# Performance work log

Measured on AMD Instinct MI355X. Metric: run time of the kernel, lower is better.

The kernel has to match this reference:

```python
import jax, jax.numpy as jnp
import numpy as np

EMB = 1024
HEADS = 16
HEAD_DIM = EMB // HEADS


def setup_inputs() -> dict:
    key = jax.random.key(0)
    ks = jax.random.split(key, 9)
    s = 1.0 / np.sqrt(EMB)
    x = jax.random.normal(ks[0], (4, 2048, EMB), dtype=jnp.float32)
    Wq = jax.random.uniform(ks[1], (EMB, EMB), minval=-s, maxval=s, dtype=jnp.float32)
    bq = jax.random.uniform(ks[2], (EMB,), minval=-s, maxval=s, dtype=jnp.float32)
    Wk = jax.random.uniform(ks[3], (EMB, EMB), minval=-s, maxval=s, dtype=jnp.float32)
    bk = jax.random.uniform(ks[4], (EMB,), minval=-s, maxval=s, dtype=jnp.float32)
    Wv = jax.random.uniform(ks[5], (EMB, EMB), minval=-s, maxval=s, dtype=jnp.float32)
    bv = jax.random.uniform(ks[6], (EMB,), minval=-s, maxval=s, dtype=jnp.float32)
    Wo = jax.random.uniform(ks[7], (EMB, EMB), minval=-s, maxval=s, dtype=jnp.float32)
    bo = jax.random.uniform(ks[8], (EMB,), minval=-s, maxval=s, dtype=jnp.float32)
    return {"x": x, "Wq": Wq, "bq": bq, "Wk": Wk, "bk": bk, "Wv": Wv, "bv": bv, "Wo": Wo, "bo": bo}


def reference(x, Wq, bq, Wk, bk, Wv, bv, Wo, bo):
    B, S, E = x.shape
    # QKV projections (torch Linear: y = x W^T + b)
    q = x @ Wq.T + bq
    k = x @ Wk.T + bk
    v = x @ Wv.T + bv
    # split heads -> [B, H, S, Dh]
    q = q.reshape(B, S, HEADS, HEAD_DIM).transpose(0, 2, 1, 3)
    k = k.reshape(B, S, HEADS, HEAD_DIM).transpose(0, 2, 1, 3)
    v = v.reshape(B, S, HEADS, HEAD_DIM).transpose(0, 2, 1, 3)
    # NOTE: module scales by 1/sqrt(emb_size), NOT 1/sqrt(head_dim)
    scale = 1.0 / jnp.sqrt(jnp.asarray(E, dtype=x.dtype))
    energy = jnp.einsum('bhqd,bhkd->bhqk', q, k) * scale
    attention = jax.nn.softmax(energy, axis=-1)
    out = jnp.einsum('bhqk,bhkd->bhqd', attention, v)
    out = out.transpose(0, 2, 1, 3).reshape(B, S, E)
    return out @ Wo.T + bo
```

## Files before the change

### kernel.cpp

```cpp
#include <hip/hip_runtime.h>


typedef __bf16 bf16;
typedef __attribute__((ext_vector_type(4))) short shortx4;
typedef __attribute__((ext_vector_type(8))) short short8;
typedef __attribute__((ext_vector_type(4))) float floatx4;
typedef __attribute__((ext_vector_type(2))) unsigned int uintx2;
typedef __attribute__((ext_vector_type(4))) unsigned int uintx4;

#define MFMA16(a, b, c) __builtin_amdgcn_mfma_f32_16x16x32_bf16((a), (b), (c), 0, 0, 0)

#define LDS_STRIDE 56

__device__ __forceinline__ float fast_exp2(float x) {
    float r;
    asm("v_exp_f32 %0, %1" : "=v"(r) : "v"(x));
    return r;
}
__device__ __forceinline__ unsigned int cvt_pk_bf16(float lo, float hi) {
    unsigned int r;
    asm("v_cvt_pk_bf16_f32 %0, %1, %2" : "=v"(r) : "v"(lo), "v"(hi));
    return r;
}

__device__ __forceinline__ void async16(const bf16* __restrict__ g, short* l) {
    __builtin_amdgcn_global_load_lds((const __attribute__((address_space(1))) void*)g,
                                     (__attribute__((address_space(3))) void*)l, 16, 0, 0);
}

__device__ __forceinline__ short8 frag8(const bf16* __restrict__ p) {
    return *(const short8*)p;
}
__device__ __forceinline__ short8 frag8(const float* __restrict__ p) {
    const floatx4 a = *(const floatx4*)p;
    const floatx4 b = *(const floatx4*)(p + 4);
    short8 r;
#pragma unroll
    for (int j = 0; j < 4; j++) {
        r[j]     = __builtin_bit_cast(short, (bf16)a[j]);
        r[4 + j] = __builtin_bit_cast(short, (bf16)b[j]);
    }
    return r;
}

__global__ __launch_bounds__(256) void convert_all(
    const float* __restrict__ x,
    const float* __restrict__ Wq, const float* __restrict__ Wk,
    const float* __restrict__ Wv, const float* __restrict__ Wo,
    bf16* __restrict__ xb, bf16* __restrict__ wb)
{
    const int bid = blockIdx.x;
    const float* src;
    short* dst;
    size_t j;
    if (bid < 4096) {
        j = (size_t)bid * 256 + threadIdx.x;
        src = x;
        dst = (short*)xb;
    } else {
        const int i = (bid - 4096) * 256 + threadIdx.x;
        const int t = i >> 17;
        j = (size_t)(i & 131071);
        src = (t == 0) ? Wq : (t == 1) ? Wk : (t == 2) ? Wv : Wo;
        dst = (short*)wb + (size_t)t * 1048576;
    }
    const floatx4 a = *(const floatx4*)(src + j * 8);
    const floatx4 b = *(const floatx4*)(src + j * 8 + 4);
    short8 r;
#pragma unroll
    for (int k = 0; k < 4; k++) {
        r[k]     = __builtin_bit_cast(short, (bf16)a[k]);
        r[4 + k] = __builtin_bit_cast(short, (bf16)b[k]);
    }
    *(short8*)(dst + j * 8) = r;
}

__global__ __launch_bounds__(256) void to_bf16(
    const float* __restrict__ in, bf16* __restrict__ out, int n8)
{
    const int i = blockIdx.x * 256 + threadIdx.x;
    if (i >= n8) return;
    const floatx4 a = *(const floatx4*)(in + (size_t)i * 8);
    const floatx4 b = *(const floatx4*)(in + (size_t)i * 8 + 4);
    short8 r;
#pragma unroll
    for (int j = 0; j < 4; j++) {
        r[j]     = __builtin_bit_cast(short, (bf16)a[j]);
        r[4 + j] = __builtin_bit_cast(short, (bf16)b[j]);
    }
    *(short8*)((short*)out + (size_t)i * 8) = r;
}

__device__ __forceinline__ void gemm128_p3(
    const bf16* __restrict__ A, const bf16* __restrict__ B,
    int m0, int n0, short* As, short* Bs, floatx4 acc[4][4])
{
    const int tid  = threadIdx.x;
    const int lane = tid & 63;
    const int w    = tid >> 6;
    const int wu   = __builtin_amdgcn_readfirstlane(w);
    const int wm   = w >> 1, wn = w & 1;
    const int g    = lane >> 4, c = lane & 15;
    const int ar   = lane >> 2;
    const int aq   = ((lane & 3) ^ (ar & 3)) * 8;
    const int aswz = (g ^ (c & 3)) * 8;

#pragma unroll
    for (int mi = 0; mi < 4; mi++)
#pragma unroll
        for (int ni = 0; ni < 4; ni++)
            acc[mi][ni] = (floatx4){0.f, 0.f, 0.f, 0.f};

    const bf16* Arow0 = A + (size_t)(m0 + w * 32 + ar) * 1024 + aq;
    const bf16* Arow1 = A + (size_t)(m0 + w * 32 + 16 + ar) * 1024 + aq;
    const bf16* Brow0 = B + (size_t)(n0 + w * 32 + ar) * 1024 + aq;
    const bf16* Brow1 = B + (size_t)(n0 + w * 32 + 16 + ar) * 1024 + aq;

    {
        short* Ad = As + wu * 1024;
        short* Bd = Bs + wu * 1024;
        async16(Arow0, Ad);        async16(Arow1, Ad + 512);
        async16(Brow0, Bd);        async16(Brow1, Bd + 512);
        async16(Arow0 + 32, Ad + 4096);  async16(Arow1 + 32, Ad + 4096 + 512);
        async16(Brow0 + 32, Bd + 4096);  async16(Brow1 + 32, Bd + 4096 + 512);
    }

    int cur = 0;
    for (int t = 0; t < 32; ++t) {
        if (t < 31) asm volatile("s_waitcnt vmcnt(4)" ::: "memory");
        else        asm volatile("s_waitcnt vmcnt(0)" ::: "memory");
        __builtin_amdgcn_sched_barrier(0);
        __builtin_amdgcn_s_barrier();
        __builtin_amdgcn_sched_barrier(0);

        const short* Ac = As + cur * 4096;
        const short* Bc = Bs + cur * 4096;
        short8 af[4], bfr[4];
#pragma unroll
        for (int mi = 0; mi < 4; mi++)
            af[mi] = *(const short8*)(Ac + (wm * 64 + mi * 16 + c) * 32 + aswz);
#pragma unroll
        for (int ni = 0; ni < 4; ni++)
            bfr[ni] = *(const short8*)(Bc + (wn * 64 + ni * 16 + c) * 32 + aswz);
#pragma unroll
        for (int mi = 0; mi < 4; mi++)
#pragma unroll
            for (int ni = 0; ni < 4; ni++)
                acc[mi][ni] = MFMA16(af[mi], bfr[ni], acc[mi][ni]);

        if (t < 30) {
            const int kn  = (t + 2) * 32;
            const int nb  = (cur == 0) ? 2 : cur - 1;
            short* Ad = As + nb * 4096 + wu * 1024;
            short* Bd = Bs + nb * 4096 + wu * 1024;
            async16(Arow0 + kn, Ad);   async16(Arow1 + kn, Ad + 512);
            async16(Brow0 + kn, Bd);   async16(Brow1 + kn, Bd + 512);
        }
        cur = (cur == 2) ? 0 : cur + 1;
    }
}

__device__ __forceinline__ void gemm128_fallback(
    const bf16* __restrict__ A, const float* __restrict__ B,
    int m0, int n0, short* As, short* Bs, floatx4 acc[4][4])
{
    const int tid  = threadIdx.x;
    const int lane = tid & 63;
    const int w    = tid >> 6;
    const int wu   = __builtin_amdgcn_readfirstlane(w);
    const int wm   = w >> 1, wn = w & 1;
    const int g    = lane >> 4, c = lane & 15;
    const int ar = lane >> 2;
    const int aq = ((lane & 3) ^ (ar & 3)) * 8;
    const int lrow = tid >> 2;
    const int lc8  = (tid & 3) * 8;

#pragma unroll
    for (int mi = 0; mi < 4; mi++)
#pragma unroll
        for (int ni = 0; ni < 4; ni++)
            acc[mi][ni] = (floatx4){0.f, 0.f, 0.f, 0.f};

    const int aswz = (g ^ (c & 3)) * 8;

    for (int k0 = 0; k0 < 1024; k0 += 32) {
        async16(A + (size_t)(m0 + w * 32 + ar) * 1024 + k0 + aq,      As + wu * 1024);
        async16(A + (size_t)(m0 + w * 32 + 16 + ar) * 1024 + k0 + aq, As + wu * 1024 + 512);
        *(short8*)(Bs + lrow * LDS_STRIDE + lc8) =
            frag8(B + (size_t)(n0 + lrow) * 1024 + k0 + lc8);
        *(short8*)(Bs + (lrow + 64) * LDS_STRIDE + lc8) =
            frag8(B + (size_t)(n0 + lrow + 64) * 1024 + k0 + lc8);
        __syncthreads();

        short8 af[4], bfr[4];
#pragma unroll
        for (int mi = 0; mi < 4; mi++)
            af[mi] = *(const short8*)(As + (wm * 64 + mi * 16 + c) * 32 + aswz);
#pragma unroll
        for (int ni = 0; ni < 4; ni++)
            bfr[ni] = *(const short8*)(Bs + (wn * 64 + ni * 16 + c) * LDS_STRIDE + g * 8);
#pragma unroll
        for (int mi = 0; mi < 4; mi++)
#pragma unroll
            for (int ni = 0; ni < 4; ni++)
                acc[mi][ni] = MFMA16(af[mi], bfr[ni], acc[mi][ni]);
        __syncthreads();
    }
}

template <typename TB>
__global__ __launch_bounds__(256) void qkv_gemm(
    const bf16* __restrict__ Xb,
    const TB* __restrict__ Wq, const TB* __restrict__ Wk, const TB* __restrict__ Wv,
    const float* __restrict__ bq, const float* __restrict__ bk, const float* __restrict__ bv,
    bf16* __restrict__ qkv)
{
    __shared__ __align__(16) short As[(sizeof(TB) == 2) ? 12288 : 4096];
    __shared__ __align__(16) short Bs[(sizeof(TB) == 2) ? 12288 : 128 * LDS_STRIDE];

    const int lin = (blockIdx.z * 64 + blockIdx.y) * 8 + blockIdx.x;
    const int xcd = lin & 7;
    const int i   = lin >> 3;
    const int z   = i >> 6;
    const int m0  = (xcd * 8 + ((i >> 3) & 7)) * 128;
    const int n0  = (i & 7) * 128;

    const TB* W       = (z == 0) ? Wq : (z == 1) ? Wk : Wv;
    const float* bias = (z == 0) ? bq : (z == 1) ? bk : bv;
    bf16* outz = qkv + (size_t)z * (8192u * 1024u);

    floatx4 acc[4][4];
    if constexpr (sizeof(TB) == 2)
        gemm128_p3(Xb, (const bf16*)W, m0, n0, As, Bs, acc);
    else
        gemm128_fallback(Xb, (const float*)W, m0, n0, As, Bs, acc);

    const int lane = threadIdx.x & 63;
    const int w = threadIdx.x >> 6;
    const int wm = w >> 1, wn = w & 1;
    const int g = lane >> 4, c = lane & 15;

    if (z == 2) {
#pragma unroll
        for (int ni = 0; ni < 4; ni++) {
            const int n = n0 + wn * 64 + ni * 16 + c;
            const float bb = bias[n];
            const int h = n >> 6, d = n & 63;
#pragma unroll
            for (int mi = 0; mi < 4; mi++) {
                const int m = m0 + wm * 64 + mi * 16 + g * 4;
                const int b = m >> 11, s = m & 2047;
                shortx4 st;
#pragma unroll
                for (int r = 0; r < 4; r++)
                    st[r] = __builtin_bit_cast(short, (bf16)(acc[mi][ni][r] + bb));
                *(shortx4*)&outz[(((size_t)((b << 4) | h)) * 64 + d) * 2048 + s] = st;
            }
        }
    } else {
#pragma unroll
        for (int ni = 0; ni < 4; ni++) {
            const int n = n0 + wn * 64 + ni * 16 + c;
            const float bb = bias[n];
            const int h = n >> 6, d = n & 63;
#pragma unroll
            for (int mi = 0; mi < 4; mi++) {
#pragma unroll
                for (int r = 0; r < 4; r++) {
                    const int m = m0 + wm * 64 + mi * 16 + g * 4 + r;
                    const int b = m >> 11, s = m & 2047;
                    outz[(((size_t)((b << 4) | h)) * 2048 + s) * 64 + d] =
                        (bf16)(acc[mi][ni][r] + bb);
                }
            }
        }
    }
}

__global__ __launch_bounds__(512, 2) void attn_kernel(
    const bf16* __restrict__ qkv, bf16* __restrict__ attn_out)
{
    __shared__ __align__(16) short Ks[2][128 * 64];
    __shared__ __align__(16) short Vs[2][64 * 128];

    const int lin  = blockIdx.y * gridDim.x + blockIdx.x;
    const int slot = lin >> 3;
    const int bh   = (lin & 7) * 8 + (slot >> 3);
    const int q0   = (slot & 7) * 256;

    const size_t HSTRIDE = 2048u * 64u;
    const bf16* __restrict__ Q  = qkv + (size_t)bh * HSTRIDE;
    const bf16* __restrict__ Kp = qkv + 8192u * 1024u + (size_t)bh * HSTRIDE;
    const bf16* __restrict__ Vt = qkv + 2u * 8192u * 1024u + (size_t)bh * HSTRIDE;

    const int tid  = threadIdx.x;
    const int lane = tid & 63;
    const int w    = tid >> 6;
    const int wu   = __builtin_amdgcn_readfirstlane(w);
    const int g    = lane >> 4, c = lane & 15;

    const float C2 = 0.04508422002778f;

    const int krow_off = lane >> 3;
    const int kchunk   = (lane & 7) ^ (lane >> 3);
    const int vrow_off = lane >> 4;
    const int vchunk   = (lane & 15) ^ ((w * 4 + (lane >> 4)) & 15);

    short8 qf[2][2];
#pragma unroll
    for (int qb = 0; qb < 2; qb++)
#pragma unroll
        for (int ks = 0; ks < 2; ks++)
            qf[qb][ks] = *(const short8*)(Q + (size_t)(q0 + w * 32 + qb * 16 + c) * 64
                                            + ks * 32 + g * 8);

    floatx4 o[2][4];
#pragma unroll
    for (int mi = 0; mi < 2; mi++)
#pragma unroll
        for (int di = 0; di < 4; di++)
            o[mi][di] = (floatx4){0.f, 0.f, 0.f, 0.f};
    float l_run[2] = {0.f, 0.f};

#pragma unroll
    for (int s = 0; s < 2; s++) {
        const int row = s * 64 + w * 8 + krow_off;
        async16(Kp + (size_t)row * 64 + kchunk * 8, &Ks[0][(s * 64 + wu * 8) * 64]);
    }
#pragma unroll
    for (int s = 0; s < 2; s++) {
        const int row = s * 32 + w * 4 + vrow_off;
        async16(Vt + (size_t)row * 2048 + vchunk * 8, &Vs[0][(s * 32 + wu * 4) * 128]);
    }
    __syncthreads();

    int cur = 0;
    for (int kb = 0; kb < 16; kb++) {
        if (kb < 15) {
            const int kn = (kb + 1) * 128;
#pragma unroll
            for (int s = 0; s < 2; s++) {
                const int row = s * 64 + w * 8 + krow_off;
                async16(Kp + (size_t)(kn + row) * 64 + kchunk * 8,
                        &Ks[cur ^ 1][(s * 64 + wu * 8) * 64]);
            }
#pragma unroll
            for (int s = 0; s < 2; s++) {
                const int row = s * 32 + w * 4 + vrow_off;
                async16(Vt + (size_t)row * 2048 + kn + vchunk * 8,
                        &Vs[cur ^ 1][(s * 32 + wu * 4) * 128]);
            }
        }

        const short* __restrict__ Kc = &Ks[cur][0];
        const short* __restrict__ Vc = &Vs[cur][0];

        floatx4 sAcc[2][8];
#pragma unroll
        for (int qb = 0; qb < 2; qb++)
#pragma unroll
            for (int ni = 0; ni < 8; ni++)
                sAcc[qb][ni] = (floatx4){0.f, 0.f, 0.f, 0.f};
#pragma unroll
        for (int ks = 0; ks < 2; ks++)
#pragma unroll
            for (int ni = 0; ni < 8; ni++) {
                const short8 kf = *(const short8*)(
                    Kc + (16 * ni + c) * 64 + (((ks * 4 + g) ^ (c & 7)) * 8));
                sAcc[0][ni] = MFMA16(kf, qf[0][ks], sAcc[0][ni]);
                sAcc[1][ni] = MFMA16(kf, qf[1][ks], sAcc[1][ni]);
            }

        unsigned int lo[2][8], hi[2][8];
#pragma unroll
        for (int qb = 0; qb < 2; qb++) {
            floatx4 sv = {0.f, 0.f, 0.f, 0.f};
#pragma unroll
            for (int ni = 0; ni < 8; ni++) {
#pragma unroll
                for (int r = 0; r < 4; r++) {
                    const float p = fast_exp2(sAcc[qb][ni][r] * C2);
                    sAcc[qb][ni][r] = p;
                    sv[r] += p;
                }
                lo[qb][ni] = cvt_pk_bf16(sAcc[qb][ni][0], sAcc[qb][ni][1]);
                hi[qb][ni] = cvt_pk_bf16(sAcc[qb][ni][2], sAcc[qb][ni][3]);
            }
            float sum = (sv[0] + sv[1]) + (sv[2] + sv[3]);
            sum += __shfl_xor(sum, 16);
            sum += __shfl_xor(sum, 32);
            l_run[qb] += sum;
        }

#pragma unroll
        for (int t = 0; t < 4; t++) {
            const short8 pf0 = __builtin_bit_cast(short8,
                (uintx4){lo[0][2 * t], hi[0][2 * t], lo[0][2 * t + 1], hi[0][2 * t + 1]});
            const short8 pf1 = __builtin_bit_cast(short8,
                (uintx4){lo[1][2 * t], hi[1][2 * t], lo[1][2 * t + 1], hi[1][2 * t + 1]});
#pragma unroll
            for (int di = 0; di < 4; di++) {
                const int rowb = (16 * di + c) * 128 + 4 * (g & 1);
                const uintx2 vlo = *(const uintx2*)(
                    Vc + rowb + (((4 * t + (g >> 1)) ^ c) * 8));
                const uintx2 vhi = *(const uintx2*)(
                    Vc + rowb + (((4 * t + 2 + (g >> 1)) ^ c) * 8));
                const short8 vf = __builtin_bit_cast(short8,
                    (uintx4){vlo[0], vlo[1], vhi[0], vhi[1]});
                o[0][di] = MFMA16(pf0, vf, o[0][di]);
                o[1][di] = MFMA16(pf1, vf, o[1][di]);
            }
        }

        if (kb < 15) __syncthreads();
        cur ^= 1;
    }

    const int b = bh >> 4, h = bh & 15;
#pragma unroll
    for (int mi = 0; mi < 2; mi++) {
#pragma unroll
        for (int r = 0; r < 4; r++) {
            const int src = (lane & 48) | (g * 4 + r);
            const float linv = 1.0f / __shfl(l_run[mi], src);
            const int srow = q0 + w * 32 + mi * 16 + g * 4 + r;
#pragma unroll
            for (int di = 0; di < 4; di++) {
                attn_out[((size_t)(b * 2048 + srow)) * 1024 + h * 64 + di * 16 + c] =
                    (bf16)(o[mi][di][r] * linv);
            }
        }
    }
}

template <typename TB>
__global__ __launch_bounds__(256) void out_gemm(
    const bf16* __restrict__ A, const TB* __restrict__ Wo,
    const float* __restrict__ bo, float* __restrict__ C)
{
    __shared__ __align__(16) short As[(sizeof(TB) == 2) ? 12288 : 4096];
    __shared__ __align__(16) short Bs[(sizeof(TB) == 2) ? 12288 : 128 * LDS_STRIDE];

    const int lin = blockIdx.y * 8 + blockIdx.x;
    const int xcd = lin & 7;
    const int i   = lin >> 3;
    const int m0  = (xcd * 8 + (i >> 3)) * 128;
    const int n0  = (i & 7) * 128;

    floatx4 acc[4][4];
    if constexpr (sizeof(TB) == 2)
        gemm128_p3(A, (const bf16*)Wo, m0, n0, As, Bs, acc);
    else
        gemm128_fallback(A, (const float*)Wo, m0, n0, As, Bs, acc);

    const int lane = threadIdx.x & 63;
    const int w = threadIdx.x >> 6;
    const int wm = w >> 1, wn = w & 1;
    const int g = lane >> 4, c = lane & 15;

#pragma unroll
    for (int ni = 0; ni < 4; ni++) {
        const int n = n0 + wn * 64 + ni * 16 + c;
        const float bb = bo[n];
#pragma unroll
        for (int mi = 0; mi < 4; mi++) {
#pragma unroll
            for (int r = 0; r < 4; r++) {
                const int m = m0 + wm * 64 + mi * 16 + g * 4 + r;
                C[(size_t)m * 1024 + n] = acc[mi][ni][r] + bb;
            }
        }
    }
}

extern "C" void kernel_launch(void* const* d_in, const int* in_sizes, int n_in,
                              void* d_out, int out_size, void* d_ws, size_t ws_size,
                              hipStream_t stream)
{
    const float* x  = (const float*)d_in[0];
    const float* Wq = (const float*)d_in[1];
    const float* bq = (const float*)d_in[2];
    const float* Wk = (const float*)d_in[3];
    const float* bk = (const float*)d_in[4];
    const float* Wv = (const float*)d_in[5];
    const float* bv = (const float*)d_in[6];
    const float* Wo = (const float*)d_in[7];
    const float* bo = (const float*)d_in[8];
    float* out = (float*)d_out;

    bf16* qkv  = (bf16*)d_ws;
    bf16* attn = qkv + 3u * 8192u * 1024u;
    bf16* xb   = attn;

    const size_t base = 64u * 1024u * 1024u;
    const bool haveW = ws_size >= base + 8u * 1024u * 1024u;
    bf16* wb = (bf16*)((char*)d_ws + base);

    if (haveW) {
        convert_all<<<dim3(6144), dim3(256), 0, stream>>>(x, Wq, Wk, Wv, Wo, xb, wb);
        qkv_gemm<bf16><<<dim3(8, 64, 3), dim3(256), 0, stream>>>(
            xb, wb, wb + 1048576u, wb + 2u * 1048576u, bq, bk, bv, qkv);
    } else {
        to_bf16<<<dim3(4096), dim3(256), 0, stream>>>(x, xb, 1048576);
        qkv_gemm<float><<<dim3(8, 64, 3), dim3(256), 0, stream>>>(
            xb, Wq, Wk, Wv, bq, bk, bv, qkv);
    }

    attn_kernel<<<dim3(8, 64), dim3(512), 0, stream>>>(qkv, attn);

    if (haveW) {
        out_gemm<bf16><<<dim3(8, 64), dim3(256), 0, stream>>>(
            attn, wb + 3u * 1048576u, bo, out);
    } else {
        out_gemm<float><<<dim3(8, 64), dim3(256), 0, stream>>>(attn, Wo, bo, out);
    }
}
```

Measured before the change: 279.9 us.

## Load weight B fragments directly from global memory instead of staging through LDS

In the bf16 GEMM path, the weight (B) tile is no longer copied into shared memory with async loads. Each wave now reads its B fragments straight from global memory in every k-step, while the A tile keeps its triple-buffered LDS pipeline. This cuts B's LDS usage and LDS traffic, which could allow more blocks per CU. The cost is that B loads are no longer prefetched ahead of use, and the two waves sharing columns each fetch them redundantly, so global or L2 latency is now exposed right before the MFMAs.

```diff
diff --git a/kernel.cpp b/kernel.cpp
--- a/kernel.cpp
+++ b/kernel.cpp
@@ -93,7 +93,7 @@
 
 __device__ __forceinline__ void gemm128_p3(
     const bf16* __restrict__ A, const bf16* __restrict__ B,
-    int m0, int n0, short* As, short* Bs, floatx4 acc[4][4])
+    int m0, int n0, short* As, floatx4 acc[4][4])
 {
     const int tid  = threadIdx.x;
     const int lane = tid & 63;
@@ -113,35 +113,32 @@
 
     const bf16* Arow0 = A + (size_t)(m0 + w * 32 + ar) * 1024 + aq;
     const bf16* Arow1 = A + (size_t)(m0 + w * 32 + 16 + ar) * 1024 + aq;
-    const bf16* Brow0 = B + (size_t)(n0 + w * 32 + ar) * 1024 + aq;
-    const bf16* Brow1 = B + (size_t)(n0 + w * 32 + 16 + ar) * 1024 + aq;
-
-    {
-        short* Ad = As + wu * 1024;
-        short* Bd = Bs + wu * 1024;
-        async16(Arow0, Ad);        async16(Arow1, Ad + 512);
-        async16(Brow0, Bd);        async16(Brow1, Bd + 512);
-        async16(Arow0 + 32, Ad + 4096);  async16(Arow1 + 32, Ad + 4096 + 512);
-        async16(Brow0 + 32, Bd + 4096);  async16(Brow1 + 32, Bd + 4096 + 512);
-    }
+    const bf16* Brow0 = B + (size_t)(n0 + wn * 64 + c) * 1024 + g * 8;
+
+    async16(Arow0,      As + wu * 1024);
+    async16(Arow1,      As + wu * 1024 + 512);
+    async16(Arow0 + 32, As + 4096 + wu * 1024);
+    async16(Arow1 + 32, As + 4096 + wu * 1024 + 512);
 
     int cur = 0;
     for (int t = 0; t < 32; ++t) {
-        if (t < 31) asm volatile("s_waitcnt vmcnt(4)" ::: "memory");
+        if (t < 31) asm volatile("s_waitcnt vmcnt(2)" ::: "memory");
         else        asm volatile("s_waitcnt vmcnt(0)" ::: "memory");
         __builtin_amdgcn_sched_barrier(0);
         __builtin_amdgcn_s_barrier();
         __builtin_amdgcn_sched_barrier(0);
 
+        const int k0 = t * 32;
+        short8 bfr[4];
+#pragma unroll
+        for (int ni = 0; ni < 4; ni++)
+            bfr[ni] = *(const short8*)(Brow0 + (size_t)(ni * 16) * 1024 + k0);
+
         const short* Ac = As + cur * 4096;
-        const short* Bc = Bs + cur * 4096;
-        short8 af[4], bfr[4];
+        short8 af[4];
 #pragma unroll
         for (int mi = 0; mi < 4; mi++)
             af[mi] = *(const short8*)(Ac + (wm * 64 + mi * 16 + c) * 32 + aswz);
-#pragma unroll
-        for (int ni = 0; ni < 4; ni++)
-            bfr[ni] = *(const short8*)(Bc + (wn * 64 + ni * 16 + c) * 32 + aswz);
 #pragma unroll
         for (int mi = 0; mi < 4; mi++)
 #pragma unroll
@@ -152,9 +149,8 @@
             const int kn  = (t + 2) * 32;
             const int nb  = (cur == 0) ? 2 : cur - 1;
             short* Ad = As + nb * 4096 + wu * 1024;
-            short* Bd = Bs + nb * 4096 + wu * 1024;
-            async16(Arow0 + kn, Ad);   async16(Arow1 + kn, Ad + 512);
-            async16(Brow0 + kn, Bd);   async16(Brow1 + kn, Bd + 512);
+            async16(Arow0 + kn, Ad);
+            async16(Arow1 + kn, Ad + 512);
         }
         cur = (cur == 2) ? 0 : cur + 1;
     }
@@ -216,7 +212,7 @@
     bf16* __restrict__ qkv)
 {
     __shared__ __align__(16) short As[(sizeof(TB) == 2) ? 12288 : 4096];
-    __shared__ __align__(16) short Bs[(sizeof(TB) == 2) ? 12288 : 128 * LDS_STRIDE];
+    __shared__ __align__(16) short Bs[(sizeof(TB) == 2) ? 8 : 128 * LDS_STRIDE];
 
     const int lin = (blockIdx.z * 64 + blockIdx.y) * 8 + blockIdx.x;
     const int xcd = lin & 7;
@@ -231,7 +227,7 @@
 
     floatx4 acc[4][4];
     if constexpr (sizeof(TB) == 2)
-        gemm128_p3(Xb, (const bf16*)W, m0, n0, As, Bs, acc);
+        gemm128_p3(Xb, (const bf16*)W, m0, n0, As, acc);
     else
         gemm128_fallback(Xb, (const float*)W, m0, n0, As, Bs, acc);
 
@@ -439,7 +435,7 @@
     const float* __restrict__ bo, float* __restrict__ C)
 {
     __shared__ __align__(16) short As[(sizeof(TB) == 2) ? 12288 : 4096];
-    __shared__ __align__(16) short Bs[(sizeof(TB) == 2) ? 12288 : 128 * LDS_STRIDE];
+    __shared__ __align__(16) short Bs[(sizeof(TB) == 2) ? 8 : 128 * LDS_STRIDE];
 
     const int lin = blockIdx.y * 8 + blockIdx.x;
     const int xcd = lin & 7;
@@ -449,7 +445,7 @@
 
     floatx4 acc[4][4];
     if constexpr (sizeof(TB) == 2)
-        gemm128_p3(A, (const bf16*)Wo, m0, n0, As, Bs, acc);
+        gemm128_p3(A, (const bf16*)Wo, m0, n0, As, acc);
     else
         gemm128_fallback(A, (const float*)Wo, m0, n0, As, Bs, acc);
 
```

Result: slower. 354.1 us (+26.5%).
